# Performance work log

Hardware: AMD Instinct MI355X
Metric: run time of the kernel (lower is better)

The kernel has to match this reference:

```python
import jax, jax.numpy as jnp
import numpy as np

EMBED_DIM = 96
OUT_DIM = 192
HEADS = 2
HEAD_DIM = OUT_DIM // HEADS  # 96
STRIDE_Q = (1, 2, 2)
STRIDE_KV = (1, 8, 8)
SCALE = 1.0 / float(np.sqrt(HEAD_DIM))


def layer_norm(x, g, b, eps=1e-5):
    m = jnp.mean(x, -1, keepdims=True)
    v = jnp.mean(jnp.square(x - m), -1, keepdims=True)
    return (x - m) * jax.lax.rsqrt(v + eps) * g + b


def pool(x, thw, conv_w, g, b, stride):
    # x: [B, heads, N, d] with cls token at position 0; depthwise conv3d pool + LayerNorm(d)
    B, nh, N, d = x.shape
    T, H, W = thw
    cls_tok, rest = x[:, :, :1], x[:, :, 1:]
    rest = rest.transpose(0, 1, 3, 2).reshape(B * nh, d, T, H, W)
    rest = jax.lax.conv_general_dilated(
        rest, conv_w, stride, [(1, 1), (1, 1), (1, 1)],
        dimension_numbers=('NCDHW', 'OIDHW', 'NCDHW'), feature_group_count=d)
    T2, H2, W2 = rest.shape[2], rest.shape[3], rest.shape[4]
    rest = rest.reshape(B, nh, d, -1).transpose(0, 1, 3, 2)
    x = jnp.concatenate([cls_tok, rest], axis=2)
    return layer_norm(x, g, b), (T2, H2, W2)


def rel_idx(q_n, k_n):
    # decomposed relative-distance indices with q/k resolution ratio scaling
    q_r = max(k_n / q_n, 1.0)
    k_r = max(q_n / k_n, 1.0)
    d = (jnp.arange(q_n, dtype=jnp.float32)[:, None] * q_r
         - jnp.arange(k_n, dtype=jnp.float32)[None, :] * k_r + (k_n - 1) * k_r)
    return d.astype(jnp.int32)


def add_rel_pos(attn, q, q_thw, k_thw, rph, rpw, rpt):
    qt, qh, qw = q_thw
    kt, kh, kw = k_thw
    Rh = rph[rel_idx(qh, kh)]  # [qh, kh, d]
    Rw = rpw[rel_idx(qw, kw)]  # [qw, kw, d]
    Rt = rpt[rel_idx(qt, kt)]  # [qt, kt, d]
    B, nh, qN, d = q.shape
    r_q = q[:, :, 1:].reshape(B, nh, qt, qh, qw, d)
    rel_h = jnp.einsum('bythwc,hkc->bythwk', r_q, Rh)  # k = kh
    rel_w = jnp.einsum('bythwc,wkc->bythwk', r_q, Rw)  # k = kw
    rel_t = jnp.einsum('bythwc,tkc->bythwk', r_q, Rt)  # k = kt
    rel = (rel_t[..., :, None, None] + rel_h[..., None, :, None]
           + rel_w[..., None, None, :]).reshape(B, nh, qt * qh * qw, kt * kh * kw)
    return attn.at[:, :, 1:, 1:].add(rel)


def _forward(x, qkv_w, qkv_b, proj_w, proj_b, pq_w, nq_g, nq_b, pk_w, nk_g, nk_b,
             pv_w, nv_g, nv_b, rel_pos_h, rel_pos_w, rel_pos_t, thw):
    B, N, C = x.shape
    qkv = (x @ qkv_w.T + qkv_b).reshape(B, N, 3, HEADS, HEAD_DIM).transpose(2, 0, 3, 1, 4)
    q, k, v = qkv[0], qkv[1], qkv[2]  # each [B, heads, N, head_dim]
    k, k_thw = pool(k, thw, pk_w, nk_g, nk_b, STRIDE_KV)
    v, _ = pool(v, thw, pv_w, nv_g, nv_b, STRIDE_KV)
    q, q_thw = pool(q, thw, pq_w, nq_g, nq_b, STRIDE_Q)
    attn = jnp.einsum('bhqd,bhkd->bhqk', q * SCALE, k)
    attn = add_rel_pos(attn, q, q_thw, k_thw, rel_pos_h, rel_pos_w, rel_pos_t)
    attn = jax.nn.softmax(attn, axis=-1)
    out = jnp.einsum('bhqk,bhkd->bhqd', attn, v) + q  # residual_pool, with cls embed
    out = out.transpose(0, 2, 1, 3).reshape(B, -1, OUT_DIM)
    return out @ proj_w.T + proj_b


def setup_inputs() -> dict:
    key = jax.random.key(0)
    ks = jax.random.split(key, 10)
    T, H, W = 8, 56, 56
    N = 1 + T * H * W  # 25089
    B = 4
    std = 0.02
    return {
        'x': jax.random.normal(ks[0], (B, N, EMBED_DIM), jnp.float32),
        'qkv_w': jax.random.normal(ks[1], (3 * OUT_DIM, EMBED_DIM), jnp.float32) * std,
        'qkv_b': jnp.zeros((3 * OUT_DIM,), jnp.float32),
        'proj_w': jax.random.normal(ks[2], (OUT_DIM, OUT_DIM), jnp.float32) * std,
        'proj_b': jnp.zeros((OUT_DIM,), jnp.float32),
        'pq_w': jax.random.normal(ks[3], (HEAD_DIM, 1, 3, 3, 3), jnp.float32) * std,
        'nq_g': jnp.ones((HEAD_DIM,), jnp.float32),
        'nq_b': jnp.zeros((HEAD_DIM,), jnp.float32),
        'pk_w': jax.random.normal(ks[4], (HEAD_DIM, 1, 3, 3, 3), jnp.float32) * std,
        'nk_g': jnp.ones((HEAD_DIM,), jnp.float32),
        'nk_b': jnp.zeros((HEAD_DIM,), jnp.float32),
        'pv_w': jax.random.normal(ks[5], (HEAD_DIM, 1, 3, 3, 3), jnp.float32) * std,
        'nv_g': jnp.ones((HEAD_DIM,), jnp.float32),
        'nv_b': jnp.zeros((HEAD_DIM,), jnp.float32),
        'rel_pos_h': jax.random.normal(ks[6], (55, HEAD_DIM), jnp.float32) * std,
        'rel_pos_w': jax.random.normal(ks[7], (55, HEAD_DIM), jnp.float32) * std,
        'rel_pos_t': jax.random.normal(ks[8], (15, HEAD_DIM), jnp.float32) * std,
        'thw_t': 8, 'thw_h': 56, 'thw_w': 56,
    }


def reference(x, qkv_w, qkv_b, proj_w, proj_b, pq_w, nq_g, nq_b, pk_w, nk_g, nk_b,
              pv_w, nv_g, nv_b, rel_pos_h, rel_pos_w, rel_pos_t, thw_t, thw_h, thw_w):
    thw = (int(thw_t), int(thw_h), int(thw_w))
    return _forward(x, qkv_w, qkv_b, proj_w, proj_b, pq_w, nq_g, nq_b, pk_w, nk_g, nk_b,
                    pv_w, nv_g, nv_b, rel_pos_h, rel_pos_w, rel_pos_t, thw)
```

## Files before the change

kernel.cpp:

```cpp
#include <hip/hip_runtime.h>
#include <hip/hip_bf16.h>

typedef short short8 __attribute__((ext_vector_type(8)));
typedef float floatx4 __attribute__((ext_vector_type(4)));
typedef float floatx4v __attribute__((ext_vector_type(4)));

#define SCALE_F 0.10206207261596575f
#define TOKSTRIDE 401424

static __device__ __forceinline__ float b2f(unsigned short u){
  unsigned int v = ((unsigned int)u) << 16; float f;
  __builtin_memcpy(&f, &v, 4); return f;
}
static __device__ __forceinline__ unsigned short f2b(float f){
  __hip_bfloat16 h = __float2bfloat16(f);
  unsigned short u; __builtin_memcpy(&u, &h, 2); return u;
}
static __device__ __forceinline__ int map20(int i){
  return (i < 2) ? i : 7 + ((i-2)/3)*8 + ((i-2)%3);
}

struct ConvDesc {
  const void* src[17];
  long long off[17];
  int count[17];
};

__global__ __launch_bounds__(256) void k_convert(ConvDesc d, unsigned short* dst_base,
                                                 int* flagp, const unsigned int* xprobe)
{
  __shared__ int sflag;
  if (threadIdx.x < 64){
    unsigned int w = xprobe[1024 + threadIdx.x];
    int e = (w >> 7) & 0xFF;
    int pl = (e >= 90 && e <= 140) ? 1 : 0;
    unsigned long long m = __ballot(pl);
    if (threadIdx.x == 0){
      sflag = (__popcll(m) < 40) ? 1 : 0;
      if (blockIdx.x == 0 && blockIdx.y == 0) *flagp = sflag;
    }
  }
  __syncthreads();
  const int flag = sflag;
  const int t = blockIdx.y + 1;
  const int cnt = d.count[t];
  unsigned short* dst = dst_base + d.off[t];
  const float* sf = (const float*)d.src[t];
  const unsigned short* su = (const unsigned short*)d.src[t];
  for (int i = blockIdx.x*blockDim.x + threadIdx.x; i < cnt; i += gridDim.x*blockDim.x){
    dst[i] = flag ? f2b(sf[i]) : su[i];
  }
}

static __device__ __forceinline__ void load_x_frag(
    const void* xr_, int flag, size_t elem_off, short8& a0, short8& a1, short8& a2)
{
  if (flag){
    const float* xr = (const float*)xr_ + elem_off;
    floatx4v f0 = *(const floatx4v*)(xr),      f1 = *(const floatx4v*)(xr+4);
    floatx4v f2 = *(const floatx4v*)(xr+32),   f3 = *(const floatx4v*)(xr+36);
    floatx4v f4 = *(const floatx4v*)(xr+64),   f5 = *(const floatx4v*)(xr+68);
    #pragma unroll
    for (int j = 0; j < 4; ++j){
      a0[j] = (short)f2b(f0[j]); a0[j+4] = (short)f2b(f1[j]);
      a1[j] = (short)f2b(f2[j]); a1[j+4] = (short)f2b(f3[j]);
      a2[j] = (short)f2b(f4[j]); a2[j+4] = (short)f2b(f5[j]);
    }
  } else {
    const unsigned short* xr = (const unsigned short*)xr_ + elem_off;
    a0 = *(const short8*)(xr);
    a1 = *(const short8*)(xr + 32);
    a2 = *(const short8*)(xr + 64);
  }
}

__global__ __launch_bounds__(256) void k_qkv(
    const void* __restrict__ x, const unsigned short* __restrict__ w,
    const unsigned short* __restrict__ bias, unsigned short* __restrict__ qr,
    unsigned short* __restrict__ kc, unsigned short* __restrict__ vc,
    unsigned short* __restrict__ kcls, unsigned short* __restrict__ vcls,
    const int* __restrict__ flagp)
{
  const int flag = *flagp;
  const int lane = threadIdx.x & 63;
  const int wv = threadIdx.x >> 6;
  const int kq = (lane >> 4) * 8;
  const int quad = lane >> 4;
  const int col_l = lane & 15;

  if (blockIdx.x < 1569){
    const int m_base = blockIdx.x * 64 + wv * 16;
    int ma = m_base + col_l; if (ma > 100355) ma = 100355;
    short8 a0, a1, a2;
    load_x_frag(x, flag, (size_t)ma*96 + kq, a0, a1, a2);

    int bbase[4], ntok[4], mrow[4];
    #pragma unroll
    for (int r = 0; r < 4; ++r){
      int m = m_base + quad*4 + r;
      mrow[r] = m;
      int bb = m / 25089;
      ntok[r] = m - bb*25089;
      bbase[r] = bb*2;
    }

    #pragma unroll
    for (int ct = 0; ct < 12; ++ct){
      int col = ct*16 + col_l;
      const unsigned short* wrow = w + col*96 + kq;
      short8 b0 = *(const short8*)(wrow);
      short8 b1 = *(const short8*)(wrow + 32);
      short8 b2 = *(const short8*)(wrow + 64);
      float bv = b2f(bias[col]);
      floatx4 acc = {0.f,0.f,0.f,0.f};
      acc = __builtin_amdgcn_mfma_f32_16x16x32_bf16(a0, b0, acc, 0,0,0);
      acc = __builtin_amdgcn_mfma_f32_16x16x32_bf16(a1, b1, acc, 0,0,0);
      acc = __builtin_amdgcn_mfma_f32_16x16x32_bf16(a2, b2, acc, 0,0,0);
      const int head = ct / 6;
      const int dt6  = ct % 6;
      #pragma unroll
      for (int r = 0; r < 4; ++r){
        if (mrow[r] < 100356)
          qr[(size_t)((bbase[r]+head)*6 + dt6)*TOKSTRIDE + (size_t)ntok[r]*16 + col_l]
            = f2b(acc[r] + bv);
      }
    }
  } else {
    const int id = blockIdx.x - 1569;
    const int isv = id / 201;
    const int bx = id - isv*201;
    const int rbase = bx * 64 + wv * 16;

    int rhoA = rbase + col_l; if (rhoA > 12803) rhoA = 12803;
    int bA, nA;
    if (rhoA < 4){ bA = rhoA; nA = 0; }
    else {
      int rp = rhoA - 4;
      bA = rp / 3200; int rem = rp - bA*3200;
      int t = rem / 400; int s = rem - t*400;
      int ry = s / 20, rx = s - ry*20;
      nA = 1 + (t*56 + map20(ry))*56 + map20(rx);
    }
    short8 a0, a1, a2;
    load_x_frag(x, flag, ((size_t)bA*25089 + nA)*96 + kq, a0, a1, a2);

    int isCls[4], bI[4], baseI[4], valid[4];
    #pragma unroll
    for (int r = 0; r < 4; ++r){
      int rho = rbase + quad*4 + r;
      valid[r] = (rho < 12804);
      if (rho > 12803) rho = 12803;
      if (rho < 4){ isCls[r] = 1; bI[r] = rho; baseI[r] = 0; }
      else {
        int rp = rho - 4;
        int b = rp / 3200; int rem = rp - b*3200;
        int t = rem / 400; int s = rem - t*400;
        int ry = s / 20, rx = s - ry*20;
        isCls[r] = 0; bI[r] = b;
        baseI[r] = (((b*8 + t)*20 + ry)*20 + rx)*192;
      }
    }

    unsigned short* buf  = isv ? vc : kc;
    unsigned short* bufc = isv ? vcls : kcls;
    #pragma unroll
    for (int ct = 0; ct < 12; ++ct){
      const int col = 192 + (isv*12 + ct)*16 + col_l;
      const unsigned short* wrow = w + col*96 + kq;
      short8 b0 = *(const short8*)(wrow);
      short8 b1 = *(const short8*)(wrow + 32);
      short8 b2 = *(const short8*)(wrow + 64);
      float bv = b2f(bias[col]);
      floatx4 acc = {0.f,0.f,0.f,0.f};
      acc = __builtin_amdgcn_mfma_f32_16x16x32_bf16(a0, b0, acc, 0,0,0);
      acc = __builtin_amdgcn_mfma_f32_16x16x32_bf16(a1, b1, acc, 0,0,0);
      acc = __builtin_amdgcn_mfma_f32_16x16x32_bf16(a2, b2, acc, 0,0,0);
      const int head = ct / 6;
      const int dstat = (ct % 6) * 16;
      #pragma unroll
      for (int r = 0; r < 4; ++r){
        if (valid[r]){
          float o = acc[r] + bv;
          if (isCls[r]) bufc[(bI[r]*2 + head)*96 + dstat + col_l] = f2b(o);
          else          buf[baseI[r] + head*96 + dstat + col_l]   = f2b(o);
        }
      }
    }
  }
}

__global__ __launch_bounds__(384) void k_pool(
    const unsigned short* __restrict__ qr, const unsigned short* __restrict__ cwq,
    const unsigned short* __restrict__ gq, const unsigned short* __restrict__ btaq,
    unsigned short* __restrict__ qp,
    const unsigned short* __restrict__ kc, const unsigned short* __restrict__ vc,
    const unsigned short* __restrict__ kcls, const unsigned short* __restrict__ vcls,
    const unsigned short* __restrict__ cwk, const unsigned short* __restrict__ gk, const unsigned short* __restrict__ bk,
    const unsigned short* __restrict__ cwv, const unsigned short* __restrict__ gv, const unsigned short* __restrict__ bv,
    unsigned short* __restrict__ kp, unsigned short* __restrict__ vt)
{
  const int tid = threadIdx.x;
  if (blockIdx.x < 1792){
    __shared__ float wlds[27*96];
    __shared__ float gls[96], bls[96];
    __shared__ float ls1[29*12], ls2[29*12];
    __shared__ float lmean[29], linvs[29];

    const int bid = blockIdx.x;
    const int y  = bid % 28;
    const int t  = (bid / 28) % 8;
    const int bh = bid / 224;
    const bool has_cls = (y == 0 && t == 0);

    for (int idx = tid; idx < 27*96; idx += 384){
      int tap = idx / 96, d = idx - tap*96;
      wlds[idx] = b2f(cwq[d*27 + tap]);
    }
    for (int idx = tid; idx < 96; idx += 384){
      gls[idx] = b2f(gq[idx]); bls[idx] = b2f(btaq[idx]);
    }
    __syncthreads();

    const int x = tid / 12, dg = tid - x*12;
    const unsigned short* rowb = qr + (size_t)(bh*6 + (dg >> 1))*TOKSTRIDE + (dg & 1)*8;
    float val[8] = {0,0,0,0,0,0,0,0};

    if (x < 28){
      #pragma unroll
      for (int dt = 0; dt < 3; ++dt){
        int tt = t + dt - 1; if (tt < 0 || tt >= 8) continue;
        #pragma unroll
        for (int dy = 0; dy < 3; ++dy){
          int yy = 2*y + dy - 1; if (yy < 0 || yy >= 56) continue;
          #pragma unroll
          for (int dx = 0; dx < 3; ++dx){
            int xv = 2*x + dx - 1; if (xv < 0 || xv >= 56) continue;
            const int tap = (dt*3+dy)*3+dx;
            short8 v = *(const short8*)(rowb + (size_t)(1 + (tt*56 + yy)*56 + xv)*16);
            const float* wr = wlds + tap*96 + dg*8;
            #pragma unroll
            for (int j = 0; j < 8; ++j) val[j] += b2f((unsigned short)v[j]) * wr[j];
          }
        }
      }
      float s1 = 0.f, s2 = 0.f;
      #pragma unroll
      for (int j = 0; j < 8; ++j){ s1 += val[j]; s2 += val[j]*val[j]; }
      ls1[x*12+dg] = s1; ls2[x*12+dg] = s2;
    } else if (has_cls && tid >= 348 && tid < 360){
      int cdg = tid - 348;
      const unsigned short* rowc = qr + (size_t)(bh*6 + (cdg >> 1))*TOKSTRIDE + (cdg & 1)*8;
      short8 v = *(const short8*)(rowc);
      float s1 = 0.f, s2 = 0.f;
      #pragma unroll
      for (int j = 0; j < 8; ++j){ val[j] = b2f((unsigned short)v[j]); s1 += val[j]; s2 += val[j]*val[j]; }
      ls1[28*12+cdg] = s1; ls2[28*12+cdg] = s2;
    }
    __syncthreads();

    if (tid < 28 || (tid == 28 && has_cls)){
      float s1 = 0.f, s2 = 0.f;
      #pragma unroll
      for (int k = 0; k < 12; ++k){ s1 += ls1[tid*12+k]; s2 += ls2[tid*12+k]; }
      float mean = s1 * (1.f/96.f);
      float var  = s2 * (1.f/96.f) - mean*mean;
      lmean[tid] = mean; linvs[tid] = rsqrtf(var + 1e-5f);
    }
    __syncthreads();

    if (x < 28){
      float mean = lmean[x], inv = linvs[x];
      int tok = 1 + (t*28 + y)*28 + x;
      short8 o;
      #pragma unroll
      for (int j = 0; j < 8; ++j)
        o[j] = (short)f2b((val[j] - mean)*inv*gls[dg*8+j] + bls[dg*8+j]);
      *(short8*)(qp + ((size_t)bh*6273 + tok)*96 + dg*8) = o;
    } else if (has_cls && tid >= 348 && tid < 360){
      int cdg = tid - 348;
      float mean = lmean[28], inv = linvs[28];
      short8 o;
      #pragma unroll
      for (int j = 0; j < 8; ++j)
        o[j] = (short)f2b((val[j] - mean)*inv*gls[cdg*8+j] + bls[cdg*8+j]);
      *(short8*)(qp + (size_t)bh*6273*96 + cdg*8) = o;
    }
  } else {
    __shared__ float r1[3][128], r2s[3][128];
    const int unit = tid >> 7;
    const int d = tid & 127;
    const int u = (blockIdx.x - 1792)*3 + unit;
    const bool live = (u < 6656);
    int isv = 0, bh = 0, key = 0;
    if (live){
      isv = u / 3328; int rem = u - isv*3328;
      bh = rem / 416; key = rem - bh*416;
    }
    const bool pad = (key >= 393);
    const int b = bh >> 1, head = bh & 1;
    const unsigned short* buf  = isv ? vc : kc;
    const unsigned short* bufc = isv ? vcls : kcls;
    const unsigned short* cw = (isv == 0) ? cwk : cwv;
    const unsigned short* g  = (isv == 0) ? gk : gv;
    const unsigned short* bt = (isv == 0) ? bk : bv;

    float val = 0.f;
    if (live && !pad && d < 96){
      if (key == 0) val = b2f(bufc[bh*96 + d]);
      else {
        int s = key - 1; int t = s / 49; int r2 = s - t*49; int y = r2 / 7; int xx = r2 - y*7;
        const unsigned short* wr = cw + d*27;
        float sum = 0.f;
        #pragma unroll
        for (int dt = 0; dt < 3; ++dt){
          int tt = t + dt - 1; if (tt < 0 || tt >= 8) continue;
          #pragma unroll
          for (int dy = 0; dy < 3; ++dy){
            if (y == 0 && dy == 0) continue;
            int ry = (y == 0) ? (dy - 1) : 2 + 3*(y-1) + dy;
            #pragma unroll
            for (int dx = 0; dx < 3; ++dx){
              if (xx == 0 && dx == 0) continue;
              int rx = (xx == 0) ? (dx - 1) : 2 + 3*(xx-1) + dx;
              sum += b2f(buf[(((b*8 + tt)*20 + ry)*20 + rx)*192 + head*96 + d]) * b2f(wr[(dt*3+dy)*3+dx]);
            }
          }
        }
        val = sum;
      }
    }
    r1[unit][d]  = (d < 96) ? val : 0.f;
    r2s[unit][d] = (d < 96) ? val*val : 0.f;
    __syncthreads();
    for (int off = 64; off > 0; off >>= 1){
      if (d < off){ r1[unit][d] += r1[unit][d+off]; r2s[unit][d] += r2s[unit][d+off]; }
      __syncthreads();
    }
    if (live && d < 96){
      float mean = r1[unit][0] * (1.f/96.f);
      float var  = r2s[unit][0] * (1.f/96.f) - mean*mean;
      float inv = rsqrtf(var + 1e-5f);
      float o = pad ? 0.f : (val - mean)*inv*b2f(g[d]) + b2f(bt[d]);
      if (isv == 0) kp[((size_t)bh*416 + key)*96 + d] = f2b(o);
      else          vt[((size_t)bh*96 + d)*416 + key] = f2b(o);
    }
  }
}

#define PSTR 424
__global__ __launch_bounds__(256) void k_attn(
    const unsigned short* __restrict__ qp, const unsigned short* __restrict__ kp,
    const unsigned short* __restrict__ vt,
    const unsigned short* __restrict__ rph, const unsigned short* __restrict__ rpw,
    const unsigned short* __restrict__ rpt,
    unsigned short* __restrict__ ao)
{
  __shared__ unsigned short P[16*PSTR];
  __shared__ __align__(16) float rel[24*16];
  __shared__ float mx_sh[4][16], sum_sh[4][16];

  const int bh = blockIdx.y;
  const int bb = bh >> 1, head = bh & 1;
  const int tid = threadIdx.x;
  const int lane = tid & 63;
  const int wv = tid >> 6;
  const int q0 = blockIdx.x * 16;

  const unsigned short* qbase = qp + (size_t)bh*6273*96;
  const unsigned short* kbase = kp + (size_t)bh*416*96;
  const unsigned short* vbase = vt + (size_t)bh*96*416;

  const int col = lane & 15;
  const int quad = lane >> 4;
  const int kq = quad * 8;

  short8 a0, a1, a2;
  {
    int qa = q0 + col; if (qa > 6272) qa = 6272;
    const unsigned short* qrow = qbase + (size_t)qa*96 + kq;
    a0 = *(const short8*)(qrow);
    a1 = *(const short8*)(qrow + 32);
    a2 = *(const short8*)(qrow + 64);
  }

  int yq4[4], xq4[4], tq4[4], livx[4], liv[4];
  #pragma unroll
  for (int r = 0; r < 4; ++r){
    int gq = q0 + quad*4 + r;
    liv[r]  = (gq >= 1);
    livx[r] = (gq >= 1 && gq <= 6272);
    int s = (gq >= 1) ? gq - 1 : 0;
    tq4[r] = s / 784; int r2 = s - tq4[r]*784; yq4[r] = r2 / 28; xq4[r] = r2 - yq4[r]*28;
  }

  #pragma unroll
  for (int j = 0; j < 2; ++j){
    const int c = (wv*2 + j)*16 + col;
    const unsigned short* rrow;
    if (c < 55)       rrow = rph + (size_t)c*96;
    else if (c < 110) rrow = rpw + (size_t)(c-55)*96;
    else { int ci = c-110; if (ci > 14) ci = 14; rrow = rpt + (size_t)ci*96; }
    rrow += kq;
    short8 b0 = *(const short8*)(rrow);
    short8 b1 = *(const short8*)(rrow + 32);
    short8 b2 = *(const short8*)(rrow + 64);
    floatx4 rc = {0.f,0.f,0.f,0.f};
    rc = __builtin_amdgcn_mfma_f32_16x16x32_bf16(a0, b0, rc, 0,0,0);
    rc = __builtin_amdgcn_mfma_f32_16x16x32_bf16(a1, b1, rc, 0,0,0);
    rc = __builtin_amdgcn_mfma_f32_16x16x32_bf16(a2, b2, rc, 0,0,0);
    #pragma unroll
    for (int r = 0; r < 4; ++r){
      if (!livx[r]) continue;
      const int m = quad*4 + r;
      if (c < 55){
        int u = yq4[r] + 24 - c;
        if (u >= 0 && u <= 24 && (u & 3) == 0) rel[(u >> 2)*16 + m] = rc[r];
      } else if (c < 110){
        int u = xq4[r] + 24 - (c - 55);
        if (u >= 0 && u <= 24 && (u & 3) == 0) rel[(8 + (u >> 2))*16 + m] = rc[r];
      } else if (c < 125){
        int u = tq4[r] + 7 - (c - 110);
        if (u >= 0 && u <= 7) rel[(16 + u)*16 + m] = rc[r];
      }
    }
  }
  __syncthreads();

  floatx4 acc[7];
  float mx[4] = {-1e30f,-1e30f,-1e30f,-1e30f};
  #pragma unroll
  for (int i = 0; i < 7; ++i){
    int t = wv*7 + i; if (t > 25) t = 25;
    const unsigned short* krow = kbase + (size_t)(t*16 + col)*96 + kq;
    short8 b0 = *(const short8*)(krow);
    short8 b1 = *(const short8*)(krow + 32);
    short8 b2 = *(const short8*)(krow + 64);
    floatx4 a = {0.f,0.f,0.f,0.f};
    a = __builtin_amdgcn_mfma_f32_16x16x32_bf16(a0, b0, a, 0,0,0);
    a = __builtin_amdgcn_mfma_f32_16x16x32_bf16(a1, b1, a, 0,0,0);
    a = __builtin_amdgcn_mfma_f32_16x16x32_bf16(a2, b2, a, 0,0,0);
    const int key = t*16 + col;
    const bool validk = (key < 393);
    int kt = 0, ky = 0, kx = 0;
    if (key >= 1 && validk){
      int ks = key - 1; kt = ks / 49; int krm = ks - kt*49; ky = krm / 7; kx = krm - ky*7;
    }
    floatx4v rh = *(const floatx4v*)(rel + ky*16 + quad*4);
    floatx4v rw = *(const floatx4v*)(rel + (8 + kx)*16 + quad*4);
    floatx4v rt = *(const floatx4v*)(rel + (16 + kt)*16 + quad*4);
    #pragma unroll
    for (int r = 0; r < 4; ++r){
      float s;
      if (!validk) s = -1e30f;
      else {
        s = a[r] * SCALE_F;
        if (key >= 1 && liv[r]) s += rh[r] + rw[r] + rt[r];
      }
      a[r] = s;
      mx[r] = fmaxf(mx[r], s);
    }
    acc[i] = a;
  }
  #pragma unroll
  for (int r = 0; r < 4; ++r){
    #pragma unroll
    for (int o = 1; o < 16; o <<= 1) mx[r] = fmaxf(mx[r], __shfl_xor(mx[r], o, 64));
  }
  if (col == 0){
    #pragma unroll
    for (int r = 0; r < 4; ++r) mx_sh[wv][quad*4 + r] = mx[r];
  }
  __syncthreads();

  float M[4];
  #pragma unroll
  for (int r = 0; r < 4; ++r){
    float m01 = fmaxf(mx_sh[0][quad*4 + r], mx_sh[1][quad*4 + r]);
    float m23 = fmaxf(mx_sh[2][quad*4 + r], mx_sh[3][quad*4 + r]);
    M[r] = fmaxf(m01, m23);
  }
  float sum[4] = {0.f,0.f,0.f,0.f};
  #pragma unroll
  for (int i = 0; i < 7; ++i){
    #pragma unroll
    for (int r = 0; r < 4; ++r){
      float e = __expf(acc[i][r] - M[r]);
      acc[i][r] = e; sum[r] += e;
    }
  }
  #pragma unroll
  for (int r = 0; r < 4; ++r){
    #pragma unroll
    for (int o = 1; o < 16; o <<= 1) sum[r] += __shfl_xor(sum[r], o, 64);
  }
  if (col == 0){
    #pragma unroll
    for (int r = 0; r < 4; ++r) sum_sh[wv][quad*4 + r] = sum[r];
  }
  #pragma unroll
  for (int i = 0; i < 7; ++i){
    int t = wv*7 + i; if (t > 25) t = 25;
    #pragma unroll
    for (int r = 0; r < 4; ++r)
      P[(quad*4 + r)*PSTR + t*16 + col] = f2b(acc[i][r]);
  }
  __syncthreads();

  float linv4[4];
  #pragma unroll
  for (int r = 0; r < 4; ++r)
    linv4[r] = 1.f / (sum_sh[0][quad*4 + r] + sum_sh[1][quad*4 + r]
                    + sum_sh[2][quad*4 + r] + sum_sh[3][quad*4 + r]);

  short8 pf[13];
  #pragma unroll
  for (int s = 0; s < 13; ++s)
    pf[s] = *(const short8*)(P + col*PSTR + s*32 + kq);

  #pragma unroll
  for (int dti = 0; dti < 2; ++dti){
    int slot = wv*2 + dti; if (slot >= 6) slot -= 6;
    const int dd = slot*16 + col;
    const unsigned short* vrow = vbase + (size_t)dd*416 + kq;
    floatx4 o = {0.f,0.f,0.f,0.f};
    #pragma unroll
    for (int s = 0; s < 13; ++s){
      short8 vf = *(const short8*)(vrow + s*32);
      o = __builtin_amdgcn_mfma_f32_16x16x32_bf16(pf[s], vf, o, 0,0,0);
    }
    #pragma unroll
    for (int r = 0; r < 4; ++r){
      int gq = q0 + quad*4 + r;
      if (gq <= 6272){
        float val = o[r] * linv4[r] + b2f(qbase[(size_t)gq*96 + dd]);
        ao[((size_t)bb*6273 + gq)*192 + head*96 + dd] = f2b(val);
      }
    }
  }
}

__global__ __launch_bounds__(256) void k_proj(
    const unsigned short* __restrict__ ao, const unsigned short* __restrict__ w,
    const unsigned short* __restrict__ bias, void* __restrict__ out, const int* __restrict__ flagp)
{
  const int flag = *flagp;
  const int lane = threadIdx.x & 63;
  const int wv = threadIdx.x >> 6;
  const int c = blockIdx.y*64 + wv*16 + (lane & 15);
  const int kq = (lane >> 4) * 8;
  short8 bfr[6];
  const unsigned short* wrow = w + c*192 + kq;
  #pragma unroll
  for (int s = 0; s < 6; ++s) bfr[s] = *(const short8*)(wrow + 32*s);
  float bv = b2f(bias[c]);
  const int m_base = blockIdx.x * 64;
  for (int i = 0; i < 4; ++i){
    int mt = m_base + i*16;
    int ma = mt + (lane & 15); if (ma > 25091) ma = 25091;
    const unsigned short* arow = ao + (size_t)ma*192 + kq;
    floatx4 acc = {0.f,0.f,0.f,0.f};
    #pragma unroll
    for (int s = 0; s < 6; ++s){
      short8 a = *(const short8*)(arow + 32*s);
      acc = __builtin_amdgcn_mfma_f32_16x16x32_bf16(a, bfr[s], acc, 0,0,0);
    }
    #pragma unroll
    for (int r = 0; r < 4; ++r){
      int m = mt + (lane >> 4)*4 + r;
      if (m < 25092){
        float o = acc[r] + bv;
        if (flag) ((float*)out)[(size_t)m*192 + c] = o;
        else      ((unsigned short*)out)[(size_t)m*192 + c] = f2b(o);
      }
    }
  }
}

extern "C" void kernel_launch(void* const* d_in, const int* in_sizes, int n_in,
                              void* d_out, int out_size, void* d_ws, size_t ws_size,
                              hipStream_t stream)
{
  char* p = (char*)d_ws;
  int* flagp = (int*)p; p += 16;
  unsigned short* conv = (unsigned short*)p;

  ConvDesc desc;
  long long cum = 0;
  for (int i = 0; i < 17; ++i){
    desc.src[i] = d_in[i];
    desc.off[i] = cum;
    desc.count[i] = in_sizes[i];
    cum += in_sizes[i];
  }
  p += (size_t)cum * 2;

  unsigned short* q_raw  = (unsigned short*)p; p += (size_t)19268352*2;
  unsigned short* kc     = (unsigned short*)p; p += (size_t)2457600*2;
  unsigned short* vc     = (unsigned short*)p; p += (size_t)2457600*2;
  unsigned short* kcls   = (unsigned short*)p; p += (size_t)768*2;
  unsigned short* vcls   = (unsigned short*)p; p += (size_t)768*2;
  unsigned short* q_pool = (unsigned short*)p; p += (size_t)4817664*2;
  unsigned short* kp_buf = (unsigned short*)p; p += (size_t)319488*2;
  unsigned short* v_t    = (unsigned short*)p; p += (size_t)319488*2;
  unsigned short* a_out  = q_raw;

  const unsigned short* cqkv_w = conv + desc.off[1];
  const unsigned short* cqkv_b = conv + desc.off[2];
  const unsigned short* cproj_w= conv + desc.off[3];
  const unsigned short* cproj_b= conv + desc.off[4];
  const unsigned short* cpq_w  = conv + desc.off[5];
  const unsigned short* cnq_g  = conv + desc.off[6];
  const unsigned short* cnq_b  = conv + desc.off[7];
  const unsigned short* cpk_w  = conv + desc.off[8];
  const unsigned short* cnk_g  = conv + desc.off[9];
  const unsigned short* cnk_b  = conv + desc.off[10];
  const unsigned short* cpv_w  = conv + desc.off[11];
  const unsigned short* cnv_g  = conv + desc.off[12];
  const unsigned short* cnv_b  = conv + desc.off[13];
  const unsigned short* crph   = conv + desc.off[14];
  const unsigned short* crpw   = conv + desc.off[15];
  const unsigned short* crpt   = conv + desc.off[16];

  k_convert<<<dim3(16, 16), 256, 0, stream>>>(desc, conv, flagp, (const unsigned int*)d_in[0]);
  k_qkv  <<<dim3(1971), 256, 0, stream>>>(d_in[0], cqkv_w, cqkv_b, q_raw, kc, vc, kcls, vcls, flagp);
  k_pool <<<dim3(4011), 384, 0, stream>>>(q_raw, cpq_w, cnq_g, cnq_b, q_pool,
                                          kc, vc, kcls, vcls,
                                          cpk_w, cnk_g, cnk_b, cpv_w, cnv_g, cnv_b, kp_buf, v_t);
  k_attn <<<dim3(393, 8), 256, 0, stream>>>(q_pool, kp_buf, v_t, crph, crpw, crpt, a_out);
  k_proj <<<dim3(393, 3), 256, 0, stream>>>(a_out, cproj_w, cproj_b, d_out, flagp);
}
```

Baseline: 265.5 us.

## Process two 16-query tiles per attention block to reuse K/V and rel-pos loads

The attention kernel now handles 32 queries per block instead of 16, so each K row and rel-pos table row fetched is reused across two MFMA query tiles, and the PV stage splits waves over query tile and head-dim slots. This halves the grid and the number of redundant K/V global reads per query. In exchange each block uses more registers and shared memory (launch bounds set to 3 blocks per CU), which could reduce occupancy or cause spills.

```diff
diff --git a/kernel.cpp b/kernel.cpp
--- a/kernel.cpp
+++ b/kernel.cpp
@@ -348,23 +348,23 @@
 }
 
 #define PSTR 424
-__global__ __launch_bounds__(256) void k_attn(
+__global__ __launch_bounds__(256, 3) void k_attn(
     const unsigned short* __restrict__ qp, const unsigned short* __restrict__ kp,
     const unsigned short* __restrict__ vt,
     const unsigned short* __restrict__ rph, const unsigned short* __restrict__ rpw,
     const unsigned short* __restrict__ rpt,
     unsigned short* __restrict__ ao)
 {
-  __shared__ unsigned short P[16*PSTR];
-  __shared__ __align__(16) float rel[24*16];
-  __shared__ float mx_sh[4][16], sum_sh[4][16];
+  __shared__ unsigned short P[32*PSTR];
+  __shared__ __align__(16) float rel[24*36 + 4];
+  __shared__ float mx_sh[4][32], sum_sh[4][32];
 
   const int bh = blockIdx.y;
   const int bb = bh >> 1, head = bh & 1;
   const int tid = threadIdx.x;
   const int lane = tid & 63;
   const int wv = tid >> 6;
-  const int q0 = blockIdx.x * 16;
+  const int q0 = blockIdx.x * 32;
 
   const unsigned short* qbase = qp + (size_t)bh*6273*96;
   const unsigned short* kbase = kp + (size_t)bh*416*96;
@@ -374,23 +374,26 @@
   const int quad = lane >> 4;
   const int kq = quad * 8;
 
-  short8 a0, a1, a2;
-  {
-    int qa = q0 + col; if (qa > 6272) qa = 6272;
+  short8 aF[2][3];
+  #pragma unroll
+  for (int tl = 0; tl < 2; ++tl){
+    int qa = q0 + tl*16 + col; if (qa > 6272) qa = 6272;
     const unsigned short* qrow = qbase + (size_t)qa*96 + kq;
-    a0 = *(const short8*)(qrow);
-    a1 = *(const short8*)(qrow + 32);
-    a2 = *(const short8*)(qrow + 64);
-  }
-
-  int yq4[4], xq4[4], tq4[4], livx[4], liv[4];
+    aF[tl][0] = *(const short8*)(qrow);
+    aF[tl][1] = *(const short8*)(qrow + 32);
+    aF[tl][2] = *(const short8*)(qrow + 64);
+  }
+
+  int yq[2][4], xq[2][4], tq[2][4], livx[2][4], liv[2][4];
+  #pragma unroll
+  for (int tl = 0; tl < 2; ++tl)
   #pragma unroll
   for (int r = 0; r < 4; ++r){
-    int gq = q0 + quad*4 + r;
-    liv[r]  = (gq >= 1);
-    livx[r] = (gq >= 1 && gq <= 6272);
+    int gq = q0 + tl*16 + quad*4 + r;
+    liv[tl][r]  = (gq >= 1);
+    livx[tl][r] = (gq >= 1 && gq <= 6272);
     int s = (gq >= 1) ? gq - 1 : 0;
-    tq4[r] = s / 784; int r2 = s - tq4[r]*784; yq4[r] = r2 / 28; xq4[r] = r2 - yq4[r]*28;
+    tq[tl][r] = s / 784; int r2 = s - tq[tl][r]*784; yq[tl][r] = r2 / 28; xq[tl][r] = r2 - yq[tl][r]*28;
   }
 
   #pragma unroll
@@ -404,30 +407,33 @@
     short8 b0 = *(const short8*)(rrow);
     short8 b1 = *(const short8*)(rrow + 32);
     short8 b2 = *(const short8*)(rrow + 64);
-    floatx4 rc = {0.f,0.f,0.f,0.f};
-    rc = __builtin_amdgcn_mfma_f32_16x16x32_bf16(a0, b0, rc, 0,0,0);
-    rc = __builtin_amdgcn_mfma_f32_16x16x32_bf16(a1, b1, rc, 0,0,0);
-    rc = __builtin_amdgcn_mfma_f32_16x16x32_bf16(a2, b2, rc, 0,0,0);
-    #pragma unroll
-    for (int r = 0; r < 4; ++r){
-      if (!livx[r]) continue;
-      const int m = quad*4 + r;
-      if (c < 55){
-        int u = yq4[r] + 24 - c;
-        if (u >= 0 && u <= 24 && (u & 3) == 0) rel[(u >> 2)*16 + m] = rc[r];
-      } else if (c < 110){
-        int u = xq4[r] + 24 - (c - 55);
-        if (u >= 0 && u <= 24 && (u & 3) == 0) rel[(8 + (u >> 2))*16 + m] = rc[r];
-      } else if (c < 125){
-        int u = tq4[r] + 7 - (c - 110);
-        if (u >= 0 && u <= 7) rel[(16 + u)*16 + m] = rc[r];
+    #pragma unroll
+    for (int tl = 0; tl < 2; ++tl){
+      floatx4 rc = {0.f,0.f,0.f,0.f};
+      rc = __builtin_amdgcn_mfma_f32_16x16x32_bf16(aF[tl][0], b0, rc, 0,0,0);
+      rc = __builtin_amdgcn_mfma_f32_16x16x32_bf16(aF[tl][1], b1, rc, 0,0,0);
+      rc = __builtin_amdgcn_mfma_f32_16x16x32_bf16(aF[tl][2], b2, rc, 0,0,0);
+      #pragma unroll
+      for (int r = 0; r < 4; ++r){
+        if (!livx[tl][r]) continue;
+        const int m = tl*16 + quad*4 + r;
+        if (c < 55){
+          int u = yq[tl][r] + 24 - c;
+          if (u >= 0 && u <= 24 && (u & 3) == 0) rel[(u >> 2)*36 + m] = rc[r];
+        } else if (c < 110){
+          int u = xq[tl][r] + 24 - (c - 55);
+          if (u >= 0 && u <= 24 && (u & 3) == 0) rel[(8 + (u >> 2))*36 + m] = rc[r];
+        } else if (c < 125){
+          int u = tq[tl][r] + 7 - (c - 110);
+          if (u >= 0 && u <= 7) rel[(16 + u)*36 + m] = rc[r];
+        }
       }
     }
   }
   __syncthreads();
 
-  floatx4 acc[7];
-  float mx[4] = {-1e30f,-1e30f,-1e30f,-1e30f};
+  floatx4 acc[2][7];
+  float mx[2][4] = {{-1e30f,-1e30f,-1e30f,-1e30f},{-1e30f,-1e30f,-1e30f,-1e30f}};
   #pragma unroll
   for (int i = 0; i < 7; ++i){
     int t = wv*7 + i; if (t > 25) t = 25;
@@ -435,91 +441,119 @@
     short8 b0 = *(const short8*)(krow);
     short8 b1 = *(const short8*)(krow + 32);
     short8 b2 = *(const short8*)(krow + 64);
-    floatx4 a = {0.f,0.f,0.f,0.f};
-    a = __builtin_amdgcn_mfma_f32_16x16x32_bf16(a0, b0, a, 0,0,0);
-    a = __builtin_amdgcn_mfma_f32_16x16x32_bf16(a1, b1, a, 0,0,0);
-    a = __builtin_amdgcn_mfma_f32_16x16x32_bf16(a2, b2, a, 0,0,0);
     const int key = t*16 + col;
     const bool validk = (key < 393);
     int kt = 0, ky = 0, kx = 0;
     if (key >= 1 && validk){
       int ks = key - 1; kt = ks / 49; int krm = ks - kt*49; ky = krm / 7; kx = krm - ky*7;
     }
-    floatx4v rh = *(const floatx4v*)(rel + ky*16 + quad*4);
-    floatx4v rw = *(const floatx4v*)(rel + (8 + kx)*16 + quad*4);
-    floatx4v rt = *(const floatx4v*)(rel + (16 + kt)*16 + quad*4);
+    floatx4v rh0 = *(const floatx4v*)(rel + ky*36 + quad*4);
+    floatx4v rh1 = *(const floatx4v*)(rel + ky*36 + 16 + quad*4);
+    floatx4v rw0 = *(const floatx4v*)(rel + (8 + kx)*36 + quad*4);
+    floatx4v rw1 = *(const floatx4v*)(rel + (8 + kx)*36 + 16 + quad*4);
+    floatx4v rt0 = *(const floatx4v*)(rel + (16 + kt)*36 + quad*4);
+    floatx4v rt1 = *(const floatx4v*)(rel + (16 + kt)*36 + 16 + quad*4);
+    #pragma unroll
+    for (int tl = 0; tl < 2; ++tl){
+      floatx4 a = {0.f,0.f,0.f,0.f};
+      a = __builtin_amdgcn_mfma_f32_16x16x32_bf16(aF[tl][0], b0, a, 0,0,0);
+      a = __builtin_amdgcn_mfma_f32_16x16x32_bf16(aF[tl][1], b1, a, 0,0,0);
+      a = __builtin_amdgcn_mfma_f32_16x16x32_bf16(aF[tl][2], b2, a, 0,0,0);
+      #pragma unroll
+      for (int r = 0; r < 4; ++r){
+        float s;
+        if (!validk) s = -1e30f;
+        else {
+          s = a[r] * SCALE_F;
+          if (key >= 1 && liv[tl][r]){
+            float rhv = tl ? rh1[r] : rh0[r];
+            float rwv = tl ? rw1[r] : rw0[r];
+            float rtv = tl ? rt1[r] : rt0[r];
+            s += rhv + rwv + rtv;
+          }
+        }
+        a[r] = s;
+        mx[tl][r] = fmaxf(mx[tl][r], s);
+      }
+      acc[tl][i] = a;
+    }
+  }
+  #pragma unroll
+  for (int tl = 0; tl < 2; ++tl)
+  #pragma unroll
+  for (int r = 0; r < 4; ++r){
+    #pragma unroll
+    for (int o = 1; o < 16; o <<= 1) mx[tl][r] = fmaxf(mx[tl][r], __shfl_xor(mx[tl][r], o, 64));
+  }
+  if (col == 0){
+    #pragma unroll
+    for (int tl = 0; tl < 2; ++tl)
+    #pragma unroll
+    for (int r = 0; r < 4; ++r) mx_sh[wv][tl*16 + quad*4 + r] = mx[tl][r];
+  }
+  __syncthreads();
+
+  float M[2][4];
+  #pragma unroll
+  for (int tl = 0; tl < 2; ++tl)
+  #pragma unroll
+  for (int r = 0; r < 4; ++r){
+    const int m = tl*16 + quad*4 + r;
+    float m01 = fmaxf(mx_sh[0][m], mx_sh[1][m]);
+    float m23 = fmaxf(mx_sh[2][m], mx_sh[3][m]);
+    M[tl][r] = fmaxf(m01, m23);
+  }
+  float sum[2][4] = {{0.f,0.f,0.f,0.f},{0.f,0.f,0.f,0.f}};
+  #pragma unroll
+  for (int i = 0; i < 7; ++i){
+    #pragma unroll
+    for (int tl = 0; tl < 2; ++tl)
     #pragma unroll
     for (int r = 0; r < 4; ++r){
-      float s;
-      if (!validk) s = -1e30f;
-      else {
-        s = a[r] * SCALE_F;
-        if (key >= 1 && liv[r]) s += rh[r] + rw[r] + rt[r];
-      }
-      a[r] = s;
-      mx[r] = fmaxf(mx[r], s);
-    }
-    acc[i] = a;
-  }
+      float e = __expf(acc[tl][i][r] - M[tl][r]);
+      acc[tl][i][r] = e; sum[tl][r] += e;
+    }
+  }
+  #pragma unroll
+  for (int tl = 0; tl < 2; ++tl)
   #pragma unroll
   for (int r = 0; r < 4; ++r){
     #pragma unroll
-    for (int o = 1; o < 16; o <<= 1) mx[r] = fmaxf(mx[r], __shfl_xor(mx[r], o, 64));
+    for (int o = 1; o < 16; o <<= 1) sum[tl][r] += __shfl_xor(sum[tl][r], o, 64);
   }
   if (col == 0){
     #pragma unroll
-    for (int r = 0; r < 4; ++r) mx_sh[wv][quad*4 + r] = mx[r];
-  }
-  __syncthreads();
-
-  float M[4];
-  #pragma unroll
-  for (int r = 0; r < 4; ++r){
-    float m01 = fmaxf(mx_sh[0][quad*4 + r], mx_sh[1][quad*4 + r]);
-    float m23 = fmaxf(mx_sh[2][quad*4 + r], mx_sh[3][quad*4 + r]);
-    M[r] = fmaxf(m01, m23);
-  }
-  float sum[4] = {0.f,0.f,0.f,0.f};
-  #pragma unroll
-  for (int i = 0; i < 7; ++i){
-    #pragma unroll
-    for (int r = 0; r < 4; ++r){
-      float e = __expf(acc[i][r] - M[r]);
-      acc[i][r] = e; sum[r] += e;
-    }
-  }
-  #pragma unroll
-  for (int r = 0; r < 4; ++r){
-    #pragma unroll
-    for (int o = 1; o < 16; o <<= 1) sum[r] += __shfl_xor(sum[r], o, 64);
-  }
-  if (col == 0){
-    #pragma unroll
-    for (int r = 0; r < 4; ++r) sum_sh[wv][quad*4 + r] = sum[r];
+    for (int tl = 0; tl < 2; ++tl)
+    #pragma unroll
+    for (int r = 0; r < 4; ++r) sum_sh[wv][tl*16 + quad*4 + r] = sum[tl][r];
   }
   #pragma unroll
   for (int i = 0; i < 7; ++i){
     int t = wv*7 + i; if (t > 25) t = 25;
     #pragma unroll
+    for (int tl = 0; tl < 2; ++tl)
+    #pragma unroll
     for (int r = 0; r < 4; ++r)
-      P[(quad*4 + r)*PSTR + t*16 + col] = f2b(acc[i][r]);
+      P[(tl*16 + quad*4 + r)*PSTR + t*16 + col] = f2b(acc[tl][i][r]);
   }
   __syncthreads();
 
+  const int tlw = wv >> 1;
   float linv4[4];
   #pragma unroll
-  for (int r = 0; r < 4; ++r)
-    linv4[r] = 1.f / (sum_sh[0][quad*4 + r] + sum_sh[1][quad*4 + r]
-                    + sum_sh[2][quad*4 + r] + sum_sh[3][quad*4 + r]);
+  for (int r = 0; r < 4; ++r){
+    const int m = tlw*16 + quad*4 + r;
+    linv4[r] = 1.f / (sum_sh[0][m] + sum_sh[1][m] + sum_sh[2][m] + sum_sh[3][m]);
+  }
 
   short8 pf[13];
   #pragma unroll
   for (int s = 0; s < 13; ++s)
-    pf[s] = *(const short8*)(P + col*PSTR + s*32 + kq);
-
-  #pragma unroll
-  for (int dti = 0; dti < 2; ++dti){
-    int slot = wv*2 + dti; if (slot >= 6) slot -= 6;
+    pf[s] = *(const short8*)(P + (tlw*16 + col)*PSTR + s*32 + kq);
+
+  #pragma unroll
+  for (int j = 0; j < 3; ++j){
+    const int slot = (wv & 1)*3 + j;
     const int dd = slot*16 + col;
     const unsigned short* vrow = vbase + (size_t)dd*416 + kq;
     floatx4 o = {0.f,0.f,0.f,0.f};
@@ -530,7 +564,7 @@
     }
     #pragma unroll
     for (int r = 0; r < 4; ++r){
-      int gq = q0 + quad*4 + r;
+      int gq = q0 + tlw*16 + quad*4 + r;
       if (gq <= 6272){
         float val = o[r] * linv4[r] + b2f(qbase[(size_t)gq*96 + dd]);
         ao[((size_t)bb*6273 + gq)*192 + head*96 + dd] = f2b(val);
@@ -626,6 +660,6 @@
   k_pool <<<dim3(4011), 384, 0, stream>>>(q_raw, cpq_w, cnq_g, cnq_b, q_pool,
                                           kc, vc, kcls, vcls,
                                           cpk_w, cnk_g, cnk_b, cpv_w, cnv_g, cnv_b, kp_buf, v_t);
-  k_attn <<<dim3(393, 8), 256, 0, stream>>>(q_pool, kp_buf, v_t, crph, crpw, crpt, a_out);
+  k_attn <<<dim3(197, 8), 256, 0, stream>>>(q_pool, kp_buf, v_t, crph, crpw, crpt, a_out);
   k_proj <<<dim3(393, 3), 256, 0, stream>>>(a_out, cproj_w, cproj_b, d_out, flagp);
 }
```

Result: no change. 264.1 us (-0.5%).
